# Kernel optimization log

Measured on AMD Instinct MI355X. Metric: run time of the kernel, lower is better.

Reference implementation:

```python
import jax, jax.numpy as jnp
import numpy as np
from jax import lax

SIGMA = 1.0
LW = int(4 * SIGMA + 0.5)  # 4 -> 9-tap kernel, matches scipy _gaussian_kernel1d
_xk = np.arange(-LW, LW + 1)
_phi = np.exp(-0.5 * _xk ** 2 / SIGMA ** 2)
GAUSS_K = (_phi / _phi.sum())[::-1].copy()
EPS = 1e-9
HIGH_T, LOW_T = 0.2, 0.1
H = W = 32


def _corr_w(x, k, mode, p):
    # x: (B,H,W); cross-correlate along last dim with 'same' output (torch Conv1d semantics)
    xp = jnp.pad(x, ((0, 0), (0, 0), (p, p)), mode=mode)
    B, Hh, L = xp.shape
    y = lax.conv_general_dilated(xp.reshape(B * Hh, 1, L), k.reshape(1, 1, -1).astype(x.dtype), (1,), 'VALID')
    return y.reshape(B, Hh, L - k.shape[0] + 1)


def _corr_h(x, k, mode, p):
    return jnp.swapaxes(_corr_w(jnp.swapaxes(x, 1, 2), k, mode, p), 1, 2)


def _gauss(x, k):
    # separable gaussian, zero padding (Conv1d padding=lw), both axes
    return _corr_w(_corr_h(x, k, 'constant', LW), k, 'constant', LW)


def _shift(m, di, dj):
    # out[i,j] = m[i+di, j+dj], zeros outside (only interior points are ever selected)
    p = jnp.pad(m, ((0, 0), (1, 1), (1, 1)))
    return p[:, 1 + di:1 + di + H, 1 + dj:1 + dj + W]


def _canny_core(x, mask, with_hyst=True):
    x = x * 0.5 + 0.5
    gray = x[:, 0] * 0.299 + x[:, 1] * 0.587 + x[:, 2] * 0.114  # (B,H,W)
    gk = jnp.asarray(GAUSS_K, gray.dtype)
    bleed = _gauss(mask[:, 0], gk)                      # (1,H,W)
    sm = _gauss(gray, gk) / (bleed + 1e-12)
    s_major = jnp.asarray([-1.0, 0.0, 1.0], sm.dtype)
    s_minor = jnp.asarray([1.0, 2.0, 1.0], sm.dtype)
    # jsobel: derivative along W then smooth along H; isobel: derivative along H then smooth along W
    jsob = _corr_h(_corr_w(sm, s_major, 'edge', 1), s_minor, 'edge', 1)
    isob = _corr_w(_corr_h(sm, s_major, 'edge', 1), s_minor, 'edge', 1)
    ai, aj = jnp.abs(isob), jnp.abs(jsob)
    mag2 = isob ** 2 + jsob ** 2
    mag = jnp.sqrt(mag2 + EPS)
    # binary_erosion of mask with full 3x3 structure, border_value=0
    mb = lax.stop_gradient(mask[0, 0]) != 0
    pm = jnp.pad(mb, 1)
    er2d = jnp.ones((H, W), bool)
    for di in (-1, 0, 1):
        for dj in (-1, 0, 1):
            er2d = er2d & pm[1 + di:1 + di + H, 1 + dj:1 + dj + W]
    # note: torch code builds eroded_mask from batch element 0 only, then reuses for all
    er = (er2d & (lax.stop_gradient(mag2[0]) > 0))[None]  # (1,H,W)
    same = ((isob >= 0) & (jsob >= 0)) | ((isob <= 0) & (jsob <= 0))
    opp = ((isob <= 0) & (jsob >= 0)) | ((isob >= 0) & (jsob <= 0))
    ai_safe = jnp.where(ai > 0, ai, jnp.asarray(1.0, ai.dtype))
    aj_safe = jnp.where(aj > 0, aj, jnp.asarray(1.0, aj.dtype))
    # (selector, w, c1_plus_shift, c2_plus_shift, c1_minus_shift, c2_minus_shift)
    octants = [
        (same & (ai >= aj), aj / (ai + EPS), (1, 0), (1, 1), (-1, 0), (-1, -1)),
        (same & (ai <= aj), ai / aj_safe, (0, 1), (1, 1), (0, -1), (-1, -1)),
        (opp & (ai <= aj), ai / aj_safe, (0, 1), (-1, 1), (0, -1), (1, -1)),
        (opp & (ai >= aj), aj / ai_safe, (-1, 0), (-1, 1), (1, 0), (1, -1)),
    ]
    lm = jnp.zeros(mag.shape, bool)
    for sel, w, p1, p2, m1, m2 in octants:
        pts = er & sel
        ip = _shift(mag, *p2) * w + _shift(mag, *p1) * (1 - w)
        im = _shift(mag, *m2) * w + _shift(mag, *m1) * (1 - w)
        lm = jnp.where(pts, (ip <= mag) & (im <= mag), lm)  # later octants overwrite, like torch
    if not with_hyst:
        return mag, None
    high = lm & (mag >= HIGH_T)
    low = lm & (mag >= LOW_T)

    def dilate(m):
        p = jnp.pad(m, ((0, 0), (1, 1), (1, 1)))
        out = jnp.zeros_like(m)
        for di in (-1, 0, 1):
            for dj in (-1, 0, 1):
                out = out | p[:, 1 + di:1 + di + H, 1 + dj:1 + dj + W]
        return out

    # hysteresis = 8-connected components of `low` that contain a `high` pixel
    def body(c):
        cur, _ = c
        return dilate(cur) & low, cur

    def cond(c):
        cur, prev = c
        return jnp.any(cur != prev)

    final, _ = lax.while_loop(cond, body, (high, jnp.zeros_like(high)))
    return mag, final


def setup_inputs() -> dict:
    key = jax.random.key(0)
    k1, _ = jax.random.split(key)
    x = jax.random.normal(k1, (8192, 3, 32, 32), dtype=jnp.float32)
    mask = jnp.ones((1, 1, 32, 32), dtype=jnp.float32)
    return {"x": x, "mask": mask}


def reference(x, mask):
    mag, final = _canny_core(x, mask, with_hyst=True)
    mf = final.astype(mag.dtype)
    out = mf + mag - lax.stop_gradient(mag)  # straight-through: value==mf, grad flows via mag
    out = (out - 0.5) / 0.5
    return out[:, None]  # (B,1,32,32)
```

## Files before the change

### kernel.cpp

```cpp
#include <hip/hip_runtime.h>
#include <math.h>

#pragma clang fp contract(off)

#define NPIX 1024

__device__ __forceinline__ void compute_gk(float gk[9]) {
    double phi[9];
    #pragma unroll
    for (int t = 0; t < 9; ++t) {
        double d = (double)(t - 4);
        phi[t] = exp(-0.5 * d * d);
    }
    double s = (((phi[0] + phi[1]) + (phi[2] + phi[3])) +
                ((phi[4] + phi[5]) + (phi[6] + phi[7]))) + phi[8];
    #pragma unroll
    for (int t = 0; t < 9; ++t) gk[t] = (float)(phi[t] / s);
}

__device__ __forceinline__ float ldz(const float* b, int i, int j) {
    return (i >= 0 && i < 32 && j >= 0 && j < 32) ? b[(i << 5) + j] : 0.0f;
}
__device__ __forceinline__ float ldc(const float* b, int i, int j) {
    i = i < 0 ? 0 : (i > 31 ? 31 : i);
    j = j < 0 ? 0 : (j > 31 ? 31 : j);
    return b[(i << 5) + j];
}

__global__ __launch_bounds__(256) void canny_pre(const float* __restrict__ x,
                                                 const float* __restrict__ mask,
                                                 float* __restrict__ ws_bleed,
                                                 unsigned int* __restrict__ ws_er,
                                                 float* __restrict__ ws_gk) {
    __shared__ float A[NPIX], Bf[NPIX], C[NPIX], D[NPIX], BL[NPIX];
    __shared__ unsigned int er32[32];
    const int tid = threadIdx.x;
    float gk[9];
    compute_gk(gk);
    if (tid < 9) ws_gk[tid] = gk[tid];

    #pragma unroll
    for (int k = 0; k < 4; ++k) { int p = tid + (k << 8); A[p] = mask[p]; }
    if (tid < 32) er32[tid] = 0u;
    __syncthreads();

    #pragma unroll
    for (int k = 0; k < 4; ++k) {
        int p = tid + (k << 8), i = p >> 5, j = p & 31;
        float s = 0.0f;
        #pragma unroll
        for (int t = 0; t < 9; ++t) s = __fmaf_rn(gk[t], ldz(A, i + t - 4, j), s);
        Bf[p] = s;
    }
    __syncthreads();
    #pragma unroll
    for (int k = 0; k < 4; ++k) {
        int p = tid + (k << 8), i = p >> 5, j = p & 31;
        float s = 0.0f;
        #pragma unroll
        for (int t = 0; t < 9; ++t) s = __fmaf_rn(gk[t], ldz(Bf, i, j + t - 4), s);
        BL[p] = s;
        ws_bleed[p] = s + 1e-12f;
    }

    bool er2d[4];
    #pragma unroll
    for (int k = 0; k < 4; ++k) {
        int p = tid + (k << 8), i = p >> 5, j = p & 31;
        bool e = true;
        for (int di = -1; di <= 1; ++di)
            for (int dj = -1; dj <= 1; ++dj) {
                int ii = i + di, jj = j + dj;
                e = e && (ii >= 0 && ii < 32 && jj >= 0 && jj < 32) && (A[(ii << 5) + jj] != 0.0f);
            }
        er2d[k] = e;
    }
    __syncthreads();

    #pragma unroll
    for (int k = 0; k < 4; ++k) {
        int p = tid + (k << 8);
        float r = x[p]            * 0.5f + 0.5f;
        float g = x[p + NPIX]     * 0.5f + 0.5f;
        float b = x[p + 2 * NPIX] * 0.5f + 0.5f;
        A[p] = r * 0.299f + g * 0.587f + b * 0.114f;
    }
    __syncthreads();
    #pragma unroll
    for (int k = 0; k < 4; ++k) {
        int p = tid + (k << 8), i = p >> 5, j = p & 31;
        float s = 0.0f;
        #pragma unroll
        for (int t = 0; t < 9; ++t) s = __fmaf_rn(gk[t], ldz(A, i + t - 4, j), s);
        Bf[p] = s;
    }
    __syncthreads();
    #pragma unroll
    for (int k = 0; k < 4; ++k) {
        int p = tid + (k << 8), i = p >> 5, j = p & 31;
        float s = 0.0f;
        #pragma unroll
        for (int t = 0; t < 9; ++t) s = __fmaf_rn(gk[t], ldz(Bf, i, j + t - 4), s);
        A[p] = s;
    }
    __syncthreads();
    #pragma unroll
    for (int k = 0; k < 4; ++k) { int p = tid + (k << 8); A[p] = A[p] / (BL[p] + 1e-12f); }
    __syncthreads();
    #pragma unroll
    for (int k = 0; k < 4; ++k) { int p = tid + (k << 8), i = p >> 5, j = p & 31;
        Bf[p] = ldc(A, i, j + 1) - ldc(A, i, j - 1); }
    __syncthreads();
    #pragma unroll
    for (int k = 0; k < 4; ++k) { int p = tid + (k << 8), i = p >> 5, j = p & 31;
        C[p] = (ldc(Bf, i - 1, j) + 2.0f * ldc(Bf, i, j)) + ldc(Bf, i + 1, j); }
    __syncthreads();
    #pragma unroll
    for (int k = 0; k < 4; ++k) { int p = tid + (k << 8), i = p >> 5, j = p & 31;
        Bf[p] = ldc(A, i + 1, j) - ldc(A, i - 1, j); }
    __syncthreads();
    #pragma unroll
    for (int k = 0; k < 4; ++k) { int p = tid + (k << 8), i = p >> 5, j = p & 31;
        D[p] = (ldc(Bf, i, j - 1) + 2.0f * ldc(Bf, i, j)) + ldc(Bf, i, j + 1); }
    __syncthreads();
    #pragma unroll
    for (int k = 0; k < 4; ++k) {
        int p = tid + (k << 8), i = p >> 5, j = p & 31;
        if (er2d[k]) {
            float m2 = D[p] * D[p] + C[p] * C[p];
            if (m2 > 0.0f) atomicOr(&er32[i], 1u << j);
        }
    }
    __syncthreads();
    if (tid < 32) ws_er[tid] = er32[tid];
}

__global__ __launch_bounds__(256) void canny_main(const float* __restrict__ x,
                                                  const float* __restrict__ ws_bleed,
                                                  const unsigned int* __restrict__ ws_er,
                                                  const float* __restrict__ ws_gk,
                                                  float* __restrict__ out) {
    __shared__ float APAD[40 * 32];
    __shared__ float BPAD[32 * 40];
    __shared__ float MPAD[34 * 34];
    __shared__ unsigned int er[32], hi32[32], lo32[32], fin32[32];
    const int tid = threadIdx.x;
    const int b = blockIdx.x;
    const int i  = tid >> 3;
    const int j0 = (tid & 7) << 2;

    float gk[9];
    #pragma unroll
    for (int t = 0; t < 9; ++t) gk[t] = ws_gk[t];

    APAD[tid < 128 ? tid : 1024 + tid] = 0.0f;
    { int r = tid >> 3, c8 = tid & 7; BPAD[r * 40 + c8 + (c8 < 4 ? 0 : 32)] = 0.0f; }
    #pragma unroll
    for (int t = 0; t < 5; ++t) { int idx = tid + (t << 8); if (idx < 34 * 34) MPAD[idx] = 0.0f; }
    if (tid < 32) er[tid] = ws_er[tid];

    {
        const float4* xr = (const float4*)(x + (size_t)b * 3 * NPIX);
        float4 r4 = xr[tid], g4 = xr[tid + 256], c4 = xr[tid + 512];
        float4 gy;
        gy.x = (r4.x * 0.5f + 0.5f) * 0.299f + (g4.x * 0.5f + 0.5f) * 0.587f + (c4.x * 0.5f + 0.5f) * 0.114f;
        gy.y = (r4.y * 0.5f + 0.5f) * 0.299f + (g4.y * 0.5f + 0.5f) * 0.587f + (c4.y * 0.5f + 0.5f) * 0.114f;
        gy.z = (r4.z * 0.5f + 0.5f) * 0.299f + (g4.z * 0.5f + 0.5f) * 0.587f + (c4.z * 0.5f + 0.5f) * 0.114f;
        gy.w = (r4.w * 0.5f + 0.5f) * 0.299f + (g4.w * 0.5f + 0.5f) * 0.587f + (c4.w * 0.5f + 0.5f) * 0.114f;
        *(float4*)&APAD[((i + 4) << 5) + j0] = gy;
    }
    __syncthreads();

    {
        float4 acc = make_float4(0.0f, 0.0f, 0.0f, 0.0f);
        #pragma unroll
        for (int t = 0; t < 9; ++t) {
            float4 v = *(const float4*)&APAD[((i + t) << 5) + j0];
            acc.x = __fmaf_rn(gk[t], v.x, acc.x);
            acc.y = __fmaf_rn(gk[t], v.y, acc.y);
            acc.z = __fmaf_rn(gk[t], v.z, acc.z);
            acc.w = __fmaf_rn(gk[t], v.w, acc.w);
        }
        *(float4*)&BPAD[i * 40 + j0 + 4] = acc;
    }
    __syncthreads();

    {
        const float* bp = &BPAD[i * 40 + j0];
        float4 w0 = *(const float4*)bp;
        float4 w1 = *(const float4*)(bp + 4);
        float4 w2 = *(const float4*)(bp + 8);
        float win[12] = {w0.x, w0.y, w0.z, w0.w, w1.x, w1.y, w1.z, w1.w,
                         w2.x, w2.y, w2.z, w2.w};
        float4 bl4 = *(const float4*)(ws_bleed + (tid << 2));
        float4 sm4;
        float s;
        s = 0.0f;
        #pragma unroll
        for (int t = 0; t < 9; ++t) s = __fmaf_rn(gk[t], win[0 + t], s);
        sm4.x = s / bl4.x;
        s = 0.0f;
        #pragma unroll
        for (int t = 0; t < 9; ++t) s = __fmaf_rn(gk[t], win[1 + t], s);
        sm4.y = s / bl4.y;
        s = 0.0f;
        #pragma unroll
        for (int t = 0; t < 9; ++t) s = __fmaf_rn(gk[t], win[2 + t], s);
        sm4.z = s / bl4.z;
        s = 0.0f;
        #pragma unroll
        for (int t = 0; t < 9; ++t) s = __fmaf_rn(gk[t], win[3 + t], s);
        sm4.w = s / bl4.w;
        *(float4*)&APAD[((i + 4) << 5) + j0] = sm4;
    }
    __syncthreads();

    float jsr[4], isr[4], mr[4];
    {
        const float* S = APAD + 128;
        const int im1 = i > 0 ? i - 1 : 0, ip1 = i < 31 ? i + 1 : 31;
        const bool le = (j0 == 0), re = (j0 == 28);
        float am[6], a0[6], ap[6];
        {
            const float* r = S + (im1 << 5) + j0 - 4;
            float4 v0 = *(const float4*)r, v1 = *(const float4*)(r + 4), v2 = *(const float4*)(r + 8);
            am[0] = le ? v1.x : v0.w; am[1] = v1.x; am[2] = v1.y; am[3] = v1.z; am[4] = v1.w;
            am[5] = re ? v1.w : v2.x;
        }
        {
            const float* r = S + (i << 5) + j0 - 4;
            float4 v0 = *(const float4*)r, v1 = *(const float4*)(r + 4), v2 = *(const float4*)(r + 8);
            a0[0] = le ? v1.x : v0.w; a0[1] = v1.x; a0[2] = v1.y; a0[3] = v1.z; a0[4] = v1.w;
            a0[5] = re ? v1.w : v2.x;
        }
        {
            const float* r = S + (ip1 << 5) + j0 - 4;
            float4 v0 = *(const float4*)r, v1 = *(const float4*)(r + 4), v2 = *(const float4*)(r + 8);
            ap[0] = le ? v1.x : v0.w; ap[1] = v1.x; ap[2] = v1.y; ap[3] = v1.z; ap[4] = v1.w;
            ap[5] = re ? v1.w : v2.x;
        }
        #pragma unroll
        for (int q = 0; q < 4; ++q) {
            float tm = am[q + 2] - am[q];
            float t0 = a0[q + 2] - a0[q];
            float tp = ap[q + 2] - ap[q];
            float jsob = (tm + 2.0f * t0) + tp;
            float um = ap[q] - am[q];
            float u0 = ap[q + 1] - am[q + 1];
            float up = ap[q + 2] - am[q + 2];
            float isob = (um + 2.0f * u0) + up;
            jsr[q] = jsob; isr[q] = isob;
            float m = sqrtf((isob * isob + jsob * jsob) + 1e-9f);
            mr[q] = m;
            MPAD[(i + 1) * 34 + (j0 + q + 1)] = m;
        }
    }
    __syncthreads();

    {
        unsigned int ew = er[i];
        unsigned int hn = 0u, ln = 0u;
        #pragma unroll
        for (int q = 0; q < 4; ++q) {
            int j = j0 + q;
            float iv = isr[q], jv = jsr[q], m = mr[q];
            float ai = fabsf(iv), aj = fabsf(jv);
            bool same = (iv >= 0.0f && jv >= 0.0f) || (iv <= 0.0f && jv <= 0.0f);
            bool opp  = (iv <= 0.0f && jv >= 0.0f) || (iv >= 0.0f && jv <= 0.0f);
            bool age  = (ai >= aj), ale = (ai <= aj);
            int oct = (opp && age) ? 3 : (opp && ale) ? 2 : (same && ale) ? 1 : 0;
            float ais = ai > 0.0f ? ai : 1.0f;
            float ajs = aj > 0.0f ? aj : 1.0f;
            float num = (oct == 3 || oct == 0) ? aj : ai;
            float den = (oct == 3) ? ais : (oct == 0) ? (ai + 1e-9f) : ajs;
            float wq = num / den;
            float omw = 1.0f - wq;
            int p2i = (oct >= 2) ? -1 : 1;
            int p1i = (oct == 0) ? 1 : (oct == 3) ? -1 : 0;
            int p1j = (oct == 1 || oct == 2) ? 1 : 0;
            int base = (i + 1) * 34 + (j + 1);
            float ipv = MPAD[base + p2i * 34 + 1] * wq + MPAD[base + p1i * 34 + p1j] * omw;
            float imv = MPAD[base - p2i * 34 - 1] * wq + MPAD[base - p1i * 34 - p1j] * omw;
            bool lm = (ipv <= m) && (imv <= m);
            bool eb = (ew >> j) & 1u;
            if (lm && eb && (m >= 0.2f)) hn |= (1u << j);
            if (lm && eb && (m >= 0.1f)) ln |= (1u << j);
        }
        #pragma unroll
        for (int mset = 1; mset < 8; mset <<= 1) {
            hn |= (unsigned int)__shfl_xor((int)hn, mset, 64);
            ln |= (unsigned int)__shfl_xor((int)ln, mset, 64);
        }
        if ((tid & 7) == 0) { hi32[i] = hn; lo32[i] = ln; }
    }
    __syncthreads();

    if (tid < 64) {
        unsigned int lw  = (tid < 32) ? lo32[tid] : 0u;
        unsigned int cur = (tid < 32) ? hi32[tid] : 0u;
        for (;;) {
            unsigned int sp  = cur | (cur << 1) | (cur >> 1);
            unsigned int upv = (unsigned int)__shfl((int)sp, (tid + 63) & 63, 64);
            if (tid == 0) upv = 0u;
            unsigned int dnv = (unsigned int)__shfl((int)sp, (tid + 1) & 63, 64);
            unsigned int nxt = (sp | upv | dnv) & lw;
            bool ch = (nxt != cur);
            cur = nxt;
            if (__ballot((int)ch) == 0ull) break;
        }
        if (tid < 32) fin32[tid] = cur;
    }
    __syncthreads();

    {
        unsigned int row = fin32[i];
        float4 o;
        o.x = ((row >> (j0    )) & 1u) ? 1.0f : -1.0f;
        o.y = ((row >> (j0 + 1)) & 1u) ? 1.0f : -1.0f;
        o.z = ((row >> (j0 + 2)) & 1u) ? 1.0f : -1.0f;
        o.w = ((row >> (j0 + 3)) & 1u) ? 1.0f : -1.0f;
        ((float4*)(out + (size_t)b * NPIX))[tid] = o;
    }
}

extern "C" void kernel_launch(void* const* d_in, const int* in_sizes, int n_in,
                              void* d_out, int out_size, void* d_ws, size_t ws_size,
                              hipStream_t stream) {
    const float* x    = (const float*)d_in[0];
    const float* mask = (const float*)d_in[1];
    float* out        = (float*)d_out;
    float* ws_bleed   = (float*)d_ws;
    unsigned int* ws_er = (unsigned int*)(ws_bleed + NPIX);
    float* ws_gk      = (float*)(ws_er + 32);
    int Bn = in_sizes[0] / (3 * NPIX);

    hipLaunchKernelGGL(canny_pre, dim3(1), dim3(256), 0, stream, x, mask, ws_bleed, ws_er, ws_gk);
    hipLaunchKernelGGL(canny_main, dim3(Bn), dim3(256), 0, stream, x, ws_bleed, ws_er, ws_gk, out);
}
```

Measured before the change: 52.71 us.

## Remove block barriers in main kernel and vectorize pre kernel

The main kernel now runs the horizontal Gaussian pass on rows the thread wrote itself, so a compiler-only memory fence replaces the block barrier there, and the smoothed image is written back in place into BPAD. Every wave now runs the hysteresis loop redundantly and broadcasts its result by shuffle, which removes the fin32 shared buffer and one more barrier. The single-block pre kernel is rewritten to use the same float4, padded-tile layout and builds the erosion bits with shuffles instead of atomics. The risk is correctness: the redundant hysteresis adds ALU work to every wave, and the barrier removal is valid only if each thread really reads only data it wrote itself.

```diff
diff --git a/kernel.cpp b/kernel.cpp
--- a/kernel.cpp
+++ b/kernel.cpp
@@ -16,15 +16,6 @@
                 ((phi[4] + phi[5]) + (phi[6] + phi[7]))) + phi[8];
     #pragma unroll
     for (int t = 0; t < 9; ++t) gk[t] = (float)(phi[t] / s);
-}
-
-__device__ __forceinline__ float ldz(const float* b, int i, int j) {
-    return (i >= 0 && i < 32 && j >= 0 && j < 32) ? b[(i << 5) + j] : 0.0f;
-}
-__device__ __forceinline__ float ldc(const float* b, int i, int j) {
-    i = i < 0 ? 0 : (i > 31 ? 31 : i);
-    j = j < 0 ? 0 : (j > 31 ? 31 : j);
-    return b[(i << 5) + j];
 }
 
 __global__ __launch_bounds__(256) void canny_pre(const float* __restrict__ x,
@@ -32,104 +23,174 @@
                                                  float* __restrict__ ws_bleed,
                                                  unsigned int* __restrict__ ws_er,
                                                  float* __restrict__ ws_gk) {
-    __shared__ float A[NPIX], Bf[NPIX], C[NPIX], D[NPIX], BL[NPIX];
+    __shared__ float APAD[40 * 32];
+    __shared__ float BPAD[32 * 40];
+    __shared__ float MPAD[34 * 34];
     __shared__ unsigned int er32[32];
     const int tid = threadIdx.x;
+    const int i  = tid >> 3;
+    const int j0 = (tid & 7) << 2;
+
     float gk[9];
     compute_gk(gk);
     if (tid < 9) ws_gk[tid] = gk[tid];
 
-    #pragma unroll
-    for (int k = 0; k < 4; ++k) { int p = tid + (k << 8); A[p] = mask[p]; }
-    if (tid < 32) er32[tid] = 0u;
-    __syncthreads();
-
-    #pragma unroll
-    for (int k = 0; k < 4; ++k) {
-        int p = tid + (k << 8), i = p >> 5, j = p & 31;
-        float s = 0.0f;
-        #pragma unroll
-        for (int t = 0; t < 9; ++t) s = __fmaf_rn(gk[t], ldz(A, i + t - 4, j), s);
-        Bf[p] = s;
-    }
-    __syncthreads();
-    #pragma unroll
-    for (int k = 0; k < 4; ++k) {
-        int p = tid + (k << 8), i = p >> 5, j = p & 31;
-        float s = 0.0f;
-        #pragma unroll
-        for (int t = 0; t < 9; ++t) s = __fmaf_rn(gk[t], ldz(Bf, i, j + t - 4), s);
-        BL[p] = s;
-        ws_bleed[p] = s + 1e-12f;
-    }
-
+    APAD[tid < 128 ? tid : 1024 + tid] = 0.0f;
+    { int r = tid >> 3, c8 = tid & 7; BPAD[r * 40 + c8 + (c8 < 4 ? 0 : 32)] = 0.0f; }
+    #pragma unroll
+    for (int t = 0; t < 5; ++t) { int idx = tid + (t << 8); if (idx < 34 * 34) MPAD[idx] = 0.0f; }
+    {
+        float4 mk = ((const float4*)mask)[tid];
+        *(float4*)&APAD[((i + 4) << 5) + j0] = mk;
+        int mbase = (i + 1) * 34 + (j0 + 1);
+        MPAD[mbase]     = mk.x;
+        MPAD[mbase + 1] = mk.y;
+        MPAD[mbase + 2] = mk.z;
+        MPAD[mbase + 3] = mk.w;
+    }
+    __syncthreads();
+
+    {
+        float4 acc = make_float4(0.0f, 0.0f, 0.0f, 0.0f);
+        #pragma unroll
+        for (int t = 0; t < 9; ++t) {
+            float4 v = *(const float4*)&APAD[((i + t) << 5) + j0];
+            acc.x = __fmaf_rn(gk[t], v.x, acc.x);
+            acc.y = __fmaf_rn(gk[t], v.y, acc.y);
+            acc.z = __fmaf_rn(gk[t], v.z, acc.z);
+            acc.w = __fmaf_rn(gk[t], v.w, acc.w);
+        }
+        *(float4*)&BPAD[i * 40 + j0 + 4] = acc;
+    }
+    asm volatile("" ::: "memory");
+
+    float bl4[4];
+    {
+        const float* bp = &BPAD[i * 40 + j0];
+        float4 w0 = *(const float4*)bp;
+        float4 w1 = *(const float4*)(bp + 4);
+        float4 w2 = *(const float4*)(bp + 8);
+        float win[12] = {w0.x, w0.y, w0.z, w0.w, w1.x, w1.y, w1.z, w1.w,
+                         w2.x, w2.y, w2.z, w2.w};
+        #pragma unroll
+        for (int q = 0; q < 4; ++q) {
+            float s = 0.0f;
+            #pragma unroll
+            for (int t = 0; t < 9; ++t) s = __fmaf_rn(gk[t], win[q + t], s);
+            bl4[q] = s + 1e-12f;
+        }
+        float4 wb = make_float4(bl4[0], bl4[1], bl4[2], bl4[3]);
+        ((float4*)ws_bleed)[tid] = wb;
+    }
     bool er2d[4];
     #pragma unroll
-    for (int k = 0; k < 4; ++k) {
-        int p = tid + (k << 8), i = p >> 5, j = p & 31;
+    for (int q = 0; q < 4; ++q) {
+        int base = (i + 1) * 34 + (j0 + q + 1);
         bool e = true;
+        #pragma unroll
         for (int di = -1; di <= 1; ++di)
-            for (int dj = -1; dj <= 1; ++dj) {
-                int ii = i + di, jj = j + dj;
-                e = e && (ii >= 0 && ii < 32 && jj >= 0 && jj < 32) && (A[(ii << 5) + jj] != 0.0f);
-            }
-        er2d[k] = e;
-    }
-    __syncthreads();
-
-    #pragma unroll
-    for (int k = 0; k < 4; ++k) {
-        int p = tid + (k << 8);
-        float r = x[p]            * 0.5f + 0.5f;
-        float g = x[p + NPIX]     * 0.5f + 0.5f;
-        float b = x[p + 2 * NPIX] * 0.5f + 0.5f;
-        A[p] = r * 0.299f + g * 0.587f + b * 0.114f;
-    }
-    __syncthreads();
-    #pragma unroll
-    for (int k = 0; k < 4; ++k) {
-        int p = tid + (k << 8), i = p >> 5, j = p & 31;
-        float s = 0.0f;
-        #pragma unroll
-        for (int t = 0; t < 9; ++t) s = __fmaf_rn(gk[t], ldz(A, i + t - 4, j), s);
-        Bf[p] = s;
-    }
-    __syncthreads();
-    #pragma unroll
-    for (int k = 0; k < 4; ++k) {
-        int p = tid + (k << 8), i = p >> 5, j = p & 31;
-        float s = 0.0f;
-        #pragma unroll
-        for (int t = 0; t < 9; ++t) s = __fmaf_rn(gk[t], ldz(Bf, i, j + t - 4), s);
-        A[p] = s;
-    }
-    __syncthreads();
-    #pragma unroll
-    for (int k = 0; k < 4; ++k) { int p = tid + (k << 8); A[p] = A[p] / (BL[p] + 1e-12f); }
-    __syncthreads();
-    #pragma unroll
-    for (int k = 0; k < 4; ++k) { int p = tid + (k << 8), i = p >> 5, j = p & 31;
-        Bf[p] = ldc(A, i, j + 1) - ldc(A, i, j - 1); }
-    __syncthreads();
-    #pragma unroll
-    for (int k = 0; k < 4; ++k) { int p = tid + (k << 8), i = p >> 5, j = p & 31;
-        C[p] = (ldc(Bf, i - 1, j) + 2.0f * ldc(Bf, i, j)) + ldc(Bf, i + 1, j); }
-    __syncthreads();
-    #pragma unroll
-    for (int k = 0; k < 4; ++k) { int p = tid + (k << 8), i = p >> 5, j = p & 31;
-        Bf[p] = ldc(A, i + 1, j) - ldc(A, i - 1, j); }
-    __syncthreads();
-    #pragma unroll
-    for (int k = 0; k < 4; ++k) { int p = tid + (k << 8), i = p >> 5, j = p & 31;
-        D[p] = (ldc(Bf, i, j - 1) + 2.0f * ldc(Bf, i, j)) + ldc(Bf, i, j + 1); }
-    __syncthreads();
-    #pragma unroll
-    for (int k = 0; k < 4; ++k) {
-        int p = tid + (k << 8), i = p >> 5, j = p & 31;
-        if (er2d[k]) {
-            float m2 = D[p] * D[p] + C[p] * C[p];
-            if (m2 > 0.0f) atomicOr(&er32[i], 1u << j);
-        }
+            #pragma unroll
+            for (int dj = -1; dj <= 1; ++dj)
+                e = e && (MPAD[base + di * 34 + dj] != 0.0f);
+        er2d[q] = e;
+    }
+    __syncthreads();
+
+    {
+        const float4* xr = (const float4*)x;
+        float4 r4 = xr[tid], g4 = xr[tid + 256], c4 = xr[tid + 512];
+        float4 gy;
+        gy.x = (r4.x * 0.5f + 0.5f) * 0.299f + (g4.x * 0.5f + 0.5f) * 0.587f + (c4.x * 0.5f + 0.5f) * 0.114f;
+        gy.y = (r4.y * 0.5f + 0.5f) * 0.299f + (g4.y * 0.5f + 0.5f) * 0.587f + (c4.y * 0.5f + 0.5f) * 0.114f;
+        gy.z = (r4.z * 0.5f + 0.5f) * 0.299f + (g4.z * 0.5f + 0.5f) * 0.587f + (c4.z * 0.5f + 0.5f) * 0.114f;
+        gy.w = (r4.w * 0.5f + 0.5f) * 0.299f + (g4.w * 0.5f + 0.5f) * 0.587f + (c4.w * 0.5f + 0.5f) * 0.114f;
+        *(float4*)&APAD[((i + 4) << 5) + j0] = gy;
+    }
+    __syncthreads();
+
+    {
+        float4 acc = make_float4(0.0f, 0.0f, 0.0f, 0.0f);
+        #pragma unroll
+        for (int t = 0; t < 9; ++t) {
+            float4 v = *(const float4*)&APAD[((i + t) << 5) + j0];
+            acc.x = __fmaf_rn(gk[t], v.x, acc.x);
+            acc.y = __fmaf_rn(gk[t], v.y, acc.y);
+            acc.z = __fmaf_rn(gk[t], v.z, acc.z);
+            acc.w = __fmaf_rn(gk[t], v.w, acc.w);
+        }
+        *(float4*)&BPAD[i * 40 + j0 + 4] = acc;
+    }
+    asm volatile("" ::: "memory");
+    {
+        const float* bp = &BPAD[i * 40 + j0];
+        float4 w0 = *(const float4*)bp;
+        float4 w1 = *(const float4*)(bp + 4);
+        float4 w2 = *(const float4*)(bp + 8);
+        float win[12] = {w0.x, w0.y, w0.z, w0.w, w1.x, w1.y, w1.z, w1.w,
+                         w2.x, w2.y, w2.z, w2.w};
+        float4 sm4;
+        float s;
+        s = 0.0f;
+        #pragma unroll
+        for (int t = 0; t < 9; ++t) s = __fmaf_rn(gk[t], win[0 + t], s);
+        sm4.x = s / bl4[0];
+        s = 0.0f;
+        #pragma unroll
+        for (int t = 0; t < 9; ++t) s = __fmaf_rn(gk[t], win[1 + t], s);
+        sm4.y = s / bl4[1];
+        s = 0.0f;
+        #pragma unroll
+        for (int t = 0; t < 9; ++t) s = __fmaf_rn(gk[t], win[2 + t], s);
+        sm4.z = s / bl4[2];
+        s = 0.0f;
+        #pragma unroll
+        for (int t = 0; t < 9; ++t) s = __fmaf_rn(gk[t], win[3 + t], s);
+        sm4.w = s / bl4[3];
+        asm volatile("" ::: "memory");
+        *(float4*)&BPAD[i * 40 + j0 + 4] = sm4;
+    }
+    __syncthreads();
+
+    {
+        const int im1 = i > 0 ? i - 1 : 0, ip1 = i < 31 ? i + 1 : 31;
+        const bool le = (j0 == 0), re = (j0 == 28);
+        float am[6], a0[6], ap[6];
+        {
+            const float* r = BPAD + im1 * 40 + j0;
+            float4 v0 = *(const float4*)r, v1 = *(const float4*)(r + 4), v2 = *(const float4*)(r + 8);
+            am[0] = le ? v1.x : v0.w; am[1] = v1.x; am[2] = v1.y; am[3] = v1.z; am[4] = v1.w;
+            am[5] = re ? v1.w : v2.x;
+        }
+        {
+            const float* r = BPAD + i * 40 + j0;
+            float4 v0 = *(const float4*)r, v1 = *(const float4*)(r + 4), v2 = *(const float4*)(r + 8);
+            a0[0] = le ? v1.x : v0.w; a0[1] = v1.x; a0[2] = v1.y; a0[3] = v1.z; a0[4] = v1.w;
+            a0[5] = re ? v1.w : v2.x;
+        }
+        {
+            const float* r = BPAD + ip1 * 40 + j0;
+            float4 v0 = *(const float4*)r, v1 = *(const float4*)(r + 4), v2 = *(const float4*)(r + 8);
+            ap[0] = le ? v1.x : v0.w; ap[1] = v1.x; ap[2] = v1.y; ap[3] = v1.z; ap[4] = v1.w;
+            ap[5] = re ? v1.w : v2.x;
+        }
+        unsigned int en = 0u;
+        #pragma unroll
+        for (int q = 0; q < 4; ++q) {
+            float tm = am[q + 2] - am[q];
+            float t0 = a0[q + 2] - a0[q];
+            float tp = ap[q + 2] - ap[q];
+            float jsob = (tm + 2.0f * t0) + tp;
+            float um = ap[q] - am[q];
+            float u0 = ap[q + 1] - am[q + 1];
+            float up = ap[q + 2] - am[q + 2];
+            float isob = (um + 2.0f * u0) + up;
+            float m2 = isob * isob + jsob * jsob;
+            if (er2d[q] && (m2 > 0.0f)) en |= (1u << (j0 + q));
+        }
+        #pragma unroll
+        for (int mset = 1; mset < 8; mset <<= 1)
+            en |= (unsigned int)__shfl_xor((int)en, mset, 64);
+        if ((tid & 7) == 0) er32[i] = en;
     }
     __syncthreads();
     if (tid < 32) ws_er[tid] = er32[tid];
@@ -143,11 +204,12 @@
     __shared__ float APAD[40 * 32];
     __shared__ float BPAD[32 * 40];
     __shared__ float MPAD[34 * 34];
-    __shared__ unsigned int er[32], hi32[32], lo32[32], fin32[32];
+    __shared__ unsigned int er[32], hi32[32], lo32[32];
     const int tid = threadIdx.x;
     const int b = blockIdx.x;
     const int i  = tid >> 3;
     const int j0 = (tid & 7) << 2;
+    const int l  = tid & 63;
 
     float gk[9];
     #pragma unroll
@@ -183,7 +245,7 @@
         }
         *(float4*)&BPAD[i * 40 + j0 + 4] = acc;
     }
-    __syncthreads();
+    asm volatile("" ::: "memory");
 
     {
         const float* bp = &BPAD[i * 40 + j0];
@@ -211,30 +273,30 @@
         #pragma unroll
         for (int t = 0; t < 9; ++t) s = __fmaf_rn(gk[t], win[3 + t], s);
         sm4.w = s / bl4.w;
-        *(float4*)&APAD[((i + 4) << 5) + j0] = sm4;
+        asm volatile("" ::: "memory");
+        *(float4*)&BPAD[i * 40 + j0 + 4] = sm4;
     }
     __syncthreads();
 
     float jsr[4], isr[4], mr[4];
     {
-        const float* S = APAD + 128;
         const int im1 = i > 0 ? i - 1 : 0, ip1 = i < 31 ? i + 1 : 31;
         const bool le = (j0 == 0), re = (j0 == 28);
         float am[6], a0[6], ap[6];
         {
-            const float* r = S + (im1 << 5) + j0 - 4;
+            const float* r = BPAD + im1 * 40 + j0;
             float4 v0 = *(const float4*)r, v1 = *(const float4*)(r + 4), v2 = *(const float4*)(r + 8);
             am[0] = le ? v1.x : v0.w; am[1] = v1.x; am[2] = v1.y; am[3] = v1.z; am[4] = v1.w;
             am[5] = re ? v1.w : v2.x;
         }
         {
-            const float* r = S + (i << 5) + j0 - 4;
+            const float* r = BPAD + i * 40 + j0;
             float4 v0 = *(const float4*)r, v1 = *(const float4*)(r + 4), v2 = *(const float4*)(r + 8);
             a0[0] = le ? v1.x : v0.w; a0[1] = v1.x; a0[2] = v1.y; a0[3] = v1.z; a0[4] = v1.w;
             a0[5] = re ? v1.w : v2.x;
         }
         {
-            const float* r = S + (ip1 << 5) + j0 - 4;
+            const float* r = BPAD + ip1 * 40 + j0;
             float4 v0 = *(const float4*)r, v1 = *(const float4*)(r + 4), v2 = *(const float4*)(r + 8);
             ap[0] = le ? v1.x : v0.w; ap[1] = v1.x; ap[2] = v1.y; ap[3] = v1.z; ap[4] = v1.w;
             ap[5] = re ? v1.w : v2.x;
@@ -295,30 +357,29 @@
     }
     __syncthreads();
 
-    if (tid < 64) {
-        unsigned int lw  = (tid < 32) ? lo32[tid] : 0u;
-        unsigned int cur = (tid < 32) ? hi32[tid] : 0u;
+    unsigned int cur;
+    {
+        unsigned int lw = (l < 32) ? lo32[l] : 0u;
+        cur             = (l < 32) ? hi32[l] : 0u;
         for (;;) {
             unsigned int sp  = cur | (cur << 1) | (cur >> 1);
-            unsigned int upv = (unsigned int)__shfl((int)sp, (tid + 63) & 63, 64);
-            if (tid == 0) upv = 0u;
-            unsigned int dnv = (unsigned int)__shfl((int)sp, (tid + 1) & 63, 64);
+            unsigned int upv = (unsigned int)__shfl((int)sp, (l + 63) & 63, 64);
+            if (l == 0) upv = 0u;
+            unsigned int dnv = (unsigned int)__shfl((int)sp, (l + 1) & 63, 64);
             unsigned int nxt = (sp | upv | dnv) & lw;
             bool ch = (nxt != cur);
             cur = nxt;
             if (__ballot((int)ch) == 0ull) break;
         }
-        if (tid < 32) fin32[tid] = cur;
-    }
-    __syncthreads();
-
-    {
-        unsigned int row = fin32[i];
+    }
+
+    {
+        unsigned int wd = (unsigned int)__shfl((int)cur, i, 64);
         float4 o;
-        o.x = ((row >> (j0    )) & 1u) ? 1.0f : -1.0f;
-        o.y = ((row >> (j0 + 1)) & 1u) ? 1.0f : -1.0f;
-        o.z = ((row >> (j0 + 2)) & 1u) ? 1.0f : -1.0f;
-        o.w = ((row >> (j0 + 3)) & 1u) ? 1.0f : -1.0f;
+        o.x = ((wd >> (j0    )) & 1u) ? 1.0f : -1.0f;
+        o.y = ((wd >> (j0 + 1)) & 1u) ? 1.0f : -1.0f;
+        o.z = ((wd >> (j0 + 2)) & 1u) ? 1.0f : -1.0f;
+        o.w = ((wd >> (j0 + 3)) & 1u) ? 1.0f : -1.0f;
         ((float4*)(out + (size_t)b * NPIX))[tid] = o;
     }
 }
```

After: 48.68 us. 7.6% less time.
